# Performance work log

Hardware: AMD Instinct MI355X
Metric: run time of the kernel (lower is better)

## Reference

```python
import jax, jax.numpy as jnp
import numpy as np

B, N, C = 2, 1024, 256
HEADS, DH = 8, 32
INNER = HEADS * DH
L, P = 3, 9
FF = 512
DEPTH = 2
KNN_K = (16, 64)
SHAPES_NP = np.array([[128, 128], [64, 64], [32, 32]], np.int32)
LEN = int((SHAPES_NP[:, 0] * SHAPES_NP[:, 1]).sum())


def _ln(x, g, b, eps=1e-5):
    m = x.mean(-1, keepdims=True)
    v = ((x - m) ** 2).mean(-1, keepdims=True)
    return (x - m) * jax.lax.rsqrt(v + eps) * g + b


def _knn_gather(x, pos, k):
    # pos: [B,N,3]; self-KNN (includes self as nearest)
    sq = jnp.sum(pos ** 2, -1)
    d2 = sq[:, :, None] + sq[:, None, :] - 2.0 * jnp.einsum('bnd,bmd->bnm', pos, pos)
    _, idx = jax.lax.top_k(-d2, k)  # [B,N,k]
    return jax.vmap(lambda xb, ib: xb[ib])(x, idx)  # [B,N,k,C]


def _self_attn_knn(x, pos3d, Wq, Wkv, Wo, bo, k):
    Bq, Nq, _ = x.shape
    knn_x = _knn_gather(x, pos3d, k)
    q = (x @ Wq).reshape(Bq, Nq, HEADS, DH)
    kk, vv = jnp.split(knn_x @ Wkv, 2, -1)
    kk = kk.reshape(Bq, Nq, k, HEADS, DH)
    vv = vv.reshape(Bq, Nq, k, HEADS, DH)
    attn = jax.nn.softmax(jnp.einsum('bnhd,bnshd->bnhs', q, kk) * (DH ** -0.5), -1)
    out = jnp.einsum('bnhs,bnshd->bnhd', attn, vv).reshape(Bq, Nq, INNER)
    return out @ Wo + bo


def _bilinear(value_l, loc, Hl, Wl):
    # value_l: [B, Hl*Wl, HEADS, DH]; loc: [B,N,HEADS,P,2] normalized [0,1]
    # grid_sample(align_corners=False, padding_mode='zeros') semantics
    Bq, Nq, Hh, Pp, _ = loc.shape
    xf = loc[..., 0] * Wl - 0.5
    yf = loc[..., 1] * Hl - 0.5
    x0 = jnp.floor(xf)
    y0 = jnp.floor(yf)
    out = jnp.zeros((Bq, Nq, Hh, Pp, DH), value_l.dtype)
    for dy in (0.0, 1.0):
        for dx in (0.0, 1.0):
            ix, iy = x0 + dx, y0 + dy
            w = (1.0 - jnp.abs(xf - ix)) * (1.0 - jnp.abs(yf - iy))
            valid = (ix >= 0) & (ix <= Wl - 1) & (iy >= 0) & (iy <= Hl - 1)
            flat = (jnp.clip(iy, 0, Hl - 1) * Wl + jnp.clip(ix, 0, Wl - 1)).astype(jnp.int32)
            flat = flat.transpose(0, 1, 3, 2).reshape(Bq, Nq * Pp, Hh)
            idx = jnp.broadcast_to(flat[..., None], (Bq, Nq * Pp, Hh, DH))
            g = jnp.take_along_axis(value_l, idx, axis=1)
            g = g.reshape(Bq, Nq, Pp, Hh, DH).transpose(0, 1, 3, 2, 4)
            out = out + g * (w * valid)[..., None]
    return out


def _msdeform(q, ref, value_src, Wval, bval, Woff, boff, Waw, baw, Wo, bo):
    Bq, Nq, _ = q.shape
    value = (value_src @ Wval + bval).reshape(Bq, -1, HEADS, DH)
    off = (q @ Woff + boff).reshape(Bq, Nq, HEADS, L, P, 2)
    aw = jax.nn.softmax((q @ Waw + baw).reshape(Bq, Nq, HEADS, L * P), -1)
    aw = aw.reshape(Bq, Nq, HEADS, L, P)
    normalizer = jnp.asarray(SHAPES_NP[:, ::-1].copy(), jnp.float32)  # (W,H) per level
    loc = ref[:, :, None, :, None, :] + off / normalizer[None, None, None, :, None, :]
    out = jnp.zeros((Bq, Nq, HEADS, DH), q.dtype)
    start = 0
    for l in range(L):
        Hl, Wl = int(SHAPES_NP[l, 0]), int(SHAPES_NP[l, 1])
        v_l = value[:, start:start + Hl * Wl]
        samp = _bilinear(v_l, loc[:, :, :, l], Hl, Wl)  # [B,N,H,P,DH]
        out = out + jnp.einsum('bnhpd,bnhp->bnhd', samp, aw[:, :, :, l])
        start += Hl * Wl
    return out.reshape(Bq, Nq, INNER) @ Wo + bo


def _forward(x, src, center_pos, center_pos3d, W_pos, b_pos, ln1_g, ln1_b, ln2_g, ln2_b, ln3_g, ln3_b,
             Wq, Wkv, Wo_sa, bo_sa, Wval, bval, Woff, boff, Waw, baw, Wo_ca, bo_ca, W1, b1, W2, b2):
    cpe = center_pos[..., 0, :] @ W_pos + b_pos  # pos_embedding(center_pos[...,0,:])
    ref = center_pos  # [B,N,L,2]
    for i in range(DEPTH):
        h = _ln(x + cpe, ln1_g[i], ln1_b[i])
        x = x + _self_attn_knn(h, center_pos3d, Wq[i], Wkv[i], Wo_sa[i], bo_sa[i], KNN_K[i])
        q = _ln(x, ln2_g[i], ln2_b[i]) + cpe  # with_pos_embed(norm(x), query_pos)
        s = _ln(src, ln2_g[i], ln2_b[i])      # PreNorm applies same LN to src
        x = x + _msdeform(q, ref, s, Wval[i], bval[i], Woff[i], boff[i], Waw[i], baw[i], Wo_ca[i], bo_ca[i])
        hf = _ln(x, ln3_g[i], ln3_b[i])
        x = x + (jax.nn.gelu(hf @ W1[i] + b1[i], approximate=False) @ W2[i] + b2[i])
    return x


def setup_inputs():
    key = jax.random.key(0)
    ks = iter(jax.random.split(key, 64))
    rn = lambda shape, s=1.0: jax.random.normal(next(ks), shape, jnp.float32) * s
    w = 0.02
    starts = np.concatenate([[0], np.cumsum(SHAPES_NP[:, 0] * SHAPES_NP[:, 1])[:-1]]).astype(np.int32)
    return {
        'x': rn((B, N, C)),
        'src': rn((B, LEN, C)),
        'center_pos': jax.random.uniform(next(ks), (B, N, L, 2), jnp.float32),
        'center_pos3d': rn((B, N, 3)),
        'spatial_shapes': jnp.asarray(SHAPES_NP),
        'level_start_index': jnp.asarray(starts),
        'W_pos': rn((2, C), w), 'b_pos': jnp.zeros((C,), jnp.float32),
        'ln1_g': jnp.ones((DEPTH, C)), 'ln1_b': jnp.zeros((DEPTH, C)),
        'ln2_g': jnp.ones((DEPTH, C)), 'ln2_b': jnp.zeros((DEPTH, C)),
        'ln3_g': jnp.ones((DEPTH, C)), 'ln3_b': jnp.zeros((DEPTH, C)),
        'Wq': rn((DEPTH, C, INNER), w), 'Wkv': rn((DEPTH, C, 2 * INNER), w),
        'Wo_sa': rn((DEPTH, INNER, C), w), 'bo_sa': jnp.zeros((DEPTH, C)),
        'Wval': rn((DEPTH, C, INNER), w), 'bval': jnp.zeros((DEPTH, INNER)),
        'Woff': rn((DEPTH, C, HEADS * L * P * 2), w), 'boff': rn((DEPTH, HEADS * L * P * 2), w),
        'Waw': rn((DEPTH, C, HEADS * L * P), w), 'baw': jnp.zeros((DEPTH, HEADS * L * P)),
        'Wo_ca': rn((DEPTH, INNER, C), w), 'bo_ca': jnp.zeros((DEPTH, C)),
        'W1': rn((DEPTH, C, FF), w), 'b1': jnp.zeros((DEPTH, FF)),
        'W2': rn((DEPTH, FF, C), w), 'b2': jnp.zeros((DEPTH, C)),
    }


def reference(x, src, center_pos, center_pos3d, spatial_shapes, level_start_index, W_pos, b_pos,
              ln1_g, ln1_b, ln2_g, ln2_b, ln3_g, ln3_b, Wq, Wkv, Wo_sa, bo_sa,
              Wval, bval, Woff, boff, Waw, baw, Wo_ca, bo_ca, W1, b1, W2, b2):
    # spatial_shapes / level_start_index are fixed constants (SHAPES_NP) baked into the level loop.
    return _forward(x, src, center_pos, center_pos3d, W_pos, b_pos, ln1_g, ln1_b, ln2_g, ln2_b,
                    ln3_g, ln3_b, Wq, Wkv, Wo_sa, bo_sa, Wval, bval, Woff, boff, Waw, baw,
                    Wo_ca, bo_ca, W1, b1, W2, b2)
```

## Files before the change

### kernel.cpp

```cpp
#include <hip/hip_runtime.h>
#include <math.h>


#define DEV __device__ __forceinline__

typedef __attribute__((ext_vector_type(8))) short bf16x8;
typedef __attribute__((ext_vector_type(4))) float floatx4;

DEV float gelu_f(float v) { return 0.5f * v * (1.0f + erff(v * 0.7071067811865475f)); }

DEV unsigned short f2bf(float f) {
    unsigned u = __float_as_uint(f);
    return (unsigned short)((u + 0x7fffu + ((u >> 16) & 1u)) >> 16);
}

__global__ __launch_bounds__(256) void k_lnsrc(const float* __restrict__ x, unsigned short* __restrict__ out) {
    int wid = threadIdx.x >> 6, lane = threadIdx.x & 63;
    size_t row = (size_t)blockIdx.x * 4 + wid;
    float4 v = ((const float4*)(x + row * 256))[lane];
    float s = (v.x + v.y) + (v.z + v.w);
#pragma unroll
    for (int o = 32; o; o >>= 1) s += __shfl_xor(s, o);
    float mean = s * (1.0f / 256.0f);
    float dx = v.x - mean, dy = v.y - mean, dz = v.z - mean, dw = v.w - mean;
    float q = (dx * dx + dy * dy) + (dz * dz + dw * dw);
#pragma unroll
    for (int o = 32; o; o >>= 1) q += __shfl_xor(q, o);
    float rstd = 1.0f / sqrtf(q * (1.0f / 256.0f) + 1e-5f);
    ushort4 o4;
    o4.x = f2bf(dx * rstd);
    o4.y = f2bf(dy * rstd);
    o4.z = f2bf(dz * rstd);
    o4.w = f2bf(dw * rstd);
    ((ushort4*)(out + row * 256))[lane] = o4;
}

__global__ __launch_bounds__(256) void k_lnfused(const float* __restrict__ x, const float* pre, const float* post,
                                                 const float* __restrict__ g, const float* __restrict__ b,
                                                 unsigned short* __restrict__ out) {
    int wid = threadIdx.x >> 6, lane = threadIdx.x & 63;
    size_t row = (size_t)blockIdx.x * 4 + wid;
    float4 v = ((const float4*)(x + row * 256))[lane];
    if (pre) {
        float4 p = ((const float4*)(pre + row * 256))[lane];
        v.x += p.x; v.y += p.y; v.z += p.z; v.w += p.w;
    }
    float s = (v.x + v.y) + (v.z + v.w);
#pragma unroll
    for (int o = 32; o; o >>= 1) s += __shfl_xor(s, o);
    float mean = s * (1.0f / 256.0f);
    float dx = v.x - mean, dy = v.y - mean, dz = v.z - mean, dw = v.w - mean;
    float q = (dx * dx + dy * dy) + (dz * dz + dw * dw);
#pragma unroll
    for (int o = 32; o; o >>= 1) q += __shfl_xor(q, o);
    float rstd = 1.0f / sqrtf(q * (1.0f / 256.0f) + 1e-5f);
    float4 gg = ((const float4*)g)[lane], bb = ((const float4*)b)[lane];
    float4 o4;
    o4.x = dx * rstd * gg.x + bb.x;
    o4.y = dy * rstd * gg.y + bb.y;
    o4.z = dz * rstd * gg.z + bb.z;
    o4.w = dw * rstd * gg.w + bb.w;
    if (post) {
        float4 p = ((const float4*)(post + row * 256))[lane];
        o4.x += p.x; o4.y += p.y; o4.z += p.z; o4.w += p.w;
    }
    ushort4 u4;
    u4.x = f2bf(o4.x); u4.y = f2bf(o4.y); u4.z = f2bf(o4.z); u4.w = f2bf(o4.w);
    ((ushort4*)(out + row * 256))[lane] = u4;
}

__global__ __launch_bounds__(256) void k_cpe(const float* __restrict__ cpos, const float* __restrict__ Wp,
                                             const float* __restrict__ bp, float* __restrict__ cpe) {
    int bn = blockIdx.x, c = threadIdx.x;
    float px = cpos[(size_t)bn * 6 + 0], py = cpos[(size_t)bn * 6 + 1];
    cpe[(size_t)bn * 256 + c] = px * Wp[c] + py * Wp[256 + c] + bp[c];
}

__global__ __launch_bounds__(256) void k_knn2(const float* __restrict__ pos, int* __restrict__ k16,
                                              int* __restrict__ k64) {
    __shared__ float sp[3072];
    int b = blockIdx.x >> 8;
    int n0 = (blockIdx.x & 255) * 4;
    for (int t = threadIdx.x; t < 3072; t += 256) sp[t] = pos[(size_t)b * 3072 + t];
    __syncthreads();
    int wid = threadIdx.x >> 6, lane = threadIdx.x & 63;
    int n = n0 + wid;
    float qx = sp[n * 3], qy = sp[n * 3 + 1], qz = sp[n * 3 + 2];
    float sqn = (qx * qx + qy * qy) + qz * qz;
    unsigned du[16];
#pragma unroll
    for (int t = 0; t < 16; t++) {
        int m = t * 64 + lane;
        float mx = sp[m * 3], my = sp[m * 3 + 1], mz = sp[m * 3 + 2];
        float sqm = (mx * mx + my * my) + mz * mz;
        float dt = (qx * mx + qy * my) + qz * mz;
        float d2 = (sqn + sqm) - 2.0f * dt;
        unsigned u = __float_as_uint(d2);
        du[t] = (u & 0x80000000u) ? ~u : (u | 0x80000000u);
    }
    unsigned long long lmask = (1ull << lane) - 1ull;

    auto cnt_le = [&](unsigned p) {
        int c = 0;
#pragma unroll
        for (int t = 0; t < 16; t++) c += __popcll(__ballot(du[t] <= p));
        return c;
    };
    auto find_T = [&](int K) {
        unsigned lo = 0u, hi = 0xFFFFFFFFu;
        while (lo < hi) {
            unsigned mid = lo + ((hi - lo) >> 1);
            if (cnt_le(mid) >= K) hi = mid; else lo = mid + 1;
        }
        return hi;
    };
    auto emit = [&](int K, unsigned T, int* out) {
        int base = 0;
#pragma unroll
        for (int t = 0; t < 16; t++) {
            bool lt = du[t] < T;
            unsigned long long mk = __ballot(lt);
            if (lt) out[base + __popcll(mk & lmask)] = t * 64 + lane;
            base += __popcll(mk);
        }
        int need = K - base, eb = 0;
#pragma unroll
        for (int t = 0; t < 16; t++) {
            bool eq = du[t] == T;
            unsigned long long mk = __ballot(eq);
            if (eq) {
                int r = eb + __popcll(mk & lmask);
                if (r < need) out[base + r] = t * 64 + lane;
            }
            eb += __popcll(mk);
        }
    };
    unsigned T16 = find_T(16);
    emit(16, T16, k16 + ((size_t)b * 1024 + n) * 16);
    unsigned T64 = find_T(64);
    emit(64, T64, k64 + ((size_t)b * 1024 + n) * 64);
}

template <int KK>
__global__ __launch_bounds__(256) void k_attn(const float* __restrict__ hqkv, const int* __restrict__ kidx,
                                              unsigned short* __restrict__ out) {
    int bn = blockIdx.x;
    int b = bn >> 10;
    int tid = threadIdx.x;
    __shared__ float sq[256];
    __shared__ float sa[8][KK];
    __shared__ int si[KK];
    if (tid < KK) si[tid] = kidx[(size_t)bn * KK + tid];
    sq[tid] = hqkv[(size_t)bn * 768 + tid] * 0.17677669529663689f;
    __syncthreads();
    const float* kvb = hqkv + (size_t)b * 1024 * 768;
#pragma unroll
    for (int pair = tid; pair < 8 * KK; pair += 256) {
        int s = pair & (KK - 1);
        int h = pair / KK;
        const float4* kr = (const float4*)(kvb + (size_t)si[s] * 768 + 256 + h * 32);
        const float4* q4 = (const float4*)&sq[h * 32];
        float a0 = 0.f, a1 = 0.f, a2 = 0.f, a3 = 0.f;
#pragma unroll
        for (int e = 0; e < 8; e++) {
            float4 kv = kr[e];
            float4 qv = q4[e];
            a0 = fmaf(kv.x, qv.x, a0);
            a1 = fmaf(kv.y, qv.y, a1);
            a2 = fmaf(kv.z, qv.z, a2);
            a3 = fmaf(kv.w, qv.w, a3);
        }
        sa[h][s] = (a0 + a1) + (a2 + a3);
    }
    __syncthreads();
    int h = tid >> 5, d = tid & 31;
    float mx = -1e30f;
    for (int s = d; s < KK; s += 32) mx = fmaxf(mx, sa[h][s]);
#pragma unroll
    for (int o = 16; o; o >>= 1) mx = fmaxf(mx, __shfl_xor(mx, o, 32));
    float sum = 0.0f;
    for (int s = d; s < KK; s += 32) {
        float e = __expf(sa[h][s] - mx);
        sa[h][s] = e;
        sum += e;
    }
#pragma unroll
    for (int o = 16; o; o >>= 1) sum += __shfl_xor(sum, o, 32);
    float inv = 1.0f / sum;
    __syncthreads();
    float acc = 0.0f;
    for (int s = 0; s < KK; s++) {
        float vv = kvb[(size_t)si[s] * 768 + 512 + tid];
        acc += sa[h][s] * vv;
    }
    out[(size_t)bn * 256 + tid] = f2bf(acc * inv);
}

__global__ __launch_bounds__(256) void k_msdeform(const float* __restrict__ offaw, const float* __restrict__ cpos,
                                                  const unsigned short* __restrict__ value_d,
                                                  unsigned short* __restrict__ out) {
    int bn = blockIdx.x;
    int b = bn >> 10;
    int tid = threadIdx.x;
    __shared__ float aw[216];
    __shared__ uint2 meta[864];
    __shared__ float sacc[2][256];
    if (tid < 216) aw[tid] = offaw[(size_t)bn * 648 + 432 + tid];
    __syncthreads();
    if (tid < 8) {
        float mx = -1e30f;
        for (int p = 0; p < 27; p++) mx = fmaxf(mx, aw[tid * 27 + p]);
        float s = 0.0f;
        for (int p = 0; p < 27; p++) {
            float e = __expf(aw[tid * 27 + p] - mx);
            aw[tid * 27 + p] = e;
            s += e;
        }
        float inv = 1.0f / s;
        for (int p = 0; p < 27; p++) aw[tid * 27 + p] *= inv;
    }
    __syncthreads();
    if (tid < 216) {
        int h = tid / 27, lp = tid - h * 27;
        int l = lp / 9;
        const int dims[3] = {128, 64, 32};
        const int starts[3] = {0, 16384, 20480};
        int Wl = dims[l], st = starts[l];
        float rx = cpos[(size_t)bn * 6 + l * 2], ry = cpos[(size_t)bn * 6 + l * 2 + 1];
        float ox = offaw[(size_t)bn * 648 + h * 54 + lp * 2];
        float oy = offaw[(size_t)bn * 648 + h * 54 + lp * 2 + 1];
        float rw = 1.0f / (float)Wl;
        float xf = (rx + ox * rw) * (float)Wl - 0.5f;
        float yf = (ry + oy * rw) * (float)Wl - 0.5f;
        float x0 = floorf(xf), y0 = floorf(yf);
        float wgt = aw[tid];
#pragma unroll
        for (int c = 0; c < 4; c++) {
            float ix = x0 + (float)(c & 1), iy = y0 + (float)(c >> 1);
            float w = (1.0f - fabsf(xf - ix)) * (1.0f - fabsf(yf - iy));
            bool valid = (ix >= 0.0f) & (ix <= (float)(Wl - 1)) & (iy >= 0.0f) & (iy <= (float)(Wl - 1));
            uint2 m;
            if (valid && w != 0.0f) {
                m.x = __float_as_uint(w * wgt);
                m.y = (unsigned)((st + (int)iy * Wl + (int)ix) * 1024);
            } else {
                m.x = 0u;
                m.y = 0u;
            }
            meta[tid * 4 + c] = m;
        }
    }
    __syncthreads();
    int par = tid >> 7, h2 = (tid >> 4) & 7, d2 = tid & 15;
    const char* base = (const char*)(value_d + (size_t)b * 21504 * 512) + h2 * 64 + d2 * 4;
    const uint2* mp = &meta[h2 * 108 + par * 54];
    float a0 = 0.f, a1 = 0.f;
#pragma unroll
    for (int j = 0; j < 54; j++) {
        uint2 m = mp[j];
        unsigned v = *(const unsigned*)(base + m.y);
        float w = __uint_as_float(m.x);
        a0 = fmaf(w, __uint_as_float(v << 16), a0);
        a1 = fmaf(w, __uint_as_float(v & 0xffff0000u), a1);
    }
    int ch = h2 * 32 + d2 * 2;
    sacc[par][ch] = a0;
    sacc[par][ch + 1] = a1;
    __syncthreads();
    out[(size_t)bn * 256 + tid] = f2bf(sacc[0][tid] + sacc[1][tid]);
}

struct TJobs {
    const float* src[18];
    const float* gam[18];
    unsigned short* dst[18];
    int K[18];
    int N[18];
};
__global__ __launch_bounds__(256) void k_tw(TJobs j) {
    int job = blockIdx.z;
    int K = j.K[job], N = j.N[job];
    int nt = (N + 31) >> 5, kt = K >> 5;
    if ((int)blockIdx.x >= nt || (int)blockIdx.y >= kt) return;
    __shared__ float t[32][33];
    const float* W = j.src[job];
    const float* g = j.gam[job];
    unsigned short* Wt = j.dst[job];
    int x = threadIdx.x & 31, y = threadIdx.x >> 5;
    int n0 = blockIdx.x << 5, k0 = blockIdx.y << 5;
#pragma unroll
    for (int i = 0; i < 32; i += 8) {
        int n = n0 + x;
        t[y + i][x] = (n < N) ? W[(size_t)(k0 + y + i) * N + n] : 0.0f;
    }
    __syncthreads();
    float gv = g ? g[k0 + x] : 1.0f;
#pragma unroll
    for (int i = 0; i < 32; i += 8) {
        int n = n0 + y + i;
        if (n < N) Wt[(size_t)n * K + k0 + x] = f2bf(gv * t[x][y + i]);
    }
}

__global__ __launch_bounds__(256) void k_foldval(const float* __restrict__ ln2b, const float* __restrict__ Wval,
                                                 const float* __restrict__ bval, float* __restrict__ out) {
    int d = blockIdx.x, n = threadIdx.x;
    const float* W = Wval + (size_t)d * 65536 + n;
    const float* lb = ln2b + d * 256;
    float s = bval[d * 256 + n];
    for (int k = 0; k < 256; k++) s = fmaf(lb[k], W[(size_t)k * 256], s);
    out[d * 256 + n] = s;
}

template <int BN, int WGM, int WGN, bool BIAS, bool BIAS2, bool GELUF, bool RES, bool OBF16>
__global__ __launch_bounds__(256) void k_mgemm(const unsigned short* __restrict__ A,
                                               const unsigned short* __restrict__ Bt,
                                               const float* __restrict__ bias, const float* __restrict__ bias2,
                                               int bsplit, const float* __restrict__ res, void* __restrict__ Cout,
                                               int M, int K, int Ncol) {
    constexpr int BM = 64, BK = 32;
    constexpr int WAVE_M = BM / WGM, WAVE_N = BN / WGN;
    constexpr int FM = WAVE_M / 16, FN = WAVE_N / 16;
    constexpr int BUN = BN / 64;
    __shared__ __align__(16) short a_lds[4][BM][8];
    __shared__ __align__(16) short b_lds[4][BN][8];
    int tid = threadIdx.x;
    int am0 = blockIdx.y * BM, bn0 = blockIdx.x * BN;
    int ar = tid >> 2, akc = tid & 3;
    const unsigned short* Arow = A + (size_t)(am0 + ar) * K + akc * 8;
    int4 aq;
    int4 bq[BUN];
    int nsteps = K / BK;

    auto load_tile = [&](int k0) {
        aq = *(const int4*)(Arow + k0);
#pragma unroll
        for (int jj = 0; jj < BUN; jj++) {
            int u = tid + 256 * jj;
            int col = u >> 2, kc = u & 3;
            int gn = bn0 + col;
            if (gn < Ncol)
                bq[jj] = *(const int4*)(Bt + (size_t)gn * K + k0 + kc * 8);
            else
                bq[jj] = make_int4(0, 0, 0, 0);
        }
    };
    auto write_lds = [&]() {
        *(int4*)(&a_lds[akc][ar ^ akc][0]) = aq;
#pragma unroll
        for (int jj = 0; jj < BUN; jj++) {
            int u = tid + 256 * jj;
            int col = u >> 2, kc = u & 3;
            *(int4*)(&b_lds[kc][col ^ kc][0]) = bq[jj];
        }
    };
    int lane = tid & 63, wid = tid >> 6;
    int wm = wid / WGN, wn = wid % WGN;
    int fr = lane & 15, fkc = lane >> 4;
    floatx4 acc[FM][FN] = {};

    load_tile(0);
    for (int t = 0; t < nsteps; ++t) {
        if (t) __syncthreads();
        write_lds();
        __syncthreads();
        if (t + 1 < nsteps) load_tile((t + 1) * BK);
        bf16x8 af[FM], bf[FN];
#pragma unroll
        for (int m = 0; m < FM; m++) af[m] = *(const bf16x8*)(&a_lds[fkc][(wm * WAVE_M + m * 16 + fr) ^ fkc][0]);
#pragma unroll
        for (int n = 0; n < FN; n++) bf[n] = *(const bf16x8*)(&b_lds[fkc][(wn * WAVE_N + n * 16 + fr) ^ fkc][0]);
#pragma unroll
        for (int m = 0; m < FM; m++)
#pragma unroll
            for (int n = 0; n < FN; n++)
                acc[m][n] = __builtin_amdgcn_mfma_f32_16x16x32_bf16(af[m], bf[n], acc[m][n], 0, 0, 0);
    }
    int r4 = lane >> 4;
#pragma unroll
    for (int m = 0; m < FM; m++) {
        int row = am0 + wm * WAVE_M + m * 16 + r4 * 4;
#pragma unroll
        for (int n = 0; n < FN; n++) {
            int col = bn0 + wn * WAVE_N + n * 16 + fr;
            if (col < Ncol) {
                float bsc = 0.0f;
                if (BIAS) bsc = (BIAS2 && col >= bsplit) ? bias2[col - bsplit] : bias[col];
#pragma unroll
                for (int r = 0; r < 4; r++) {
                    size_t off = (size_t)(row + r) * Ncol + col;
                    float v = acc[m][n][r] + bsc;
                    if (GELUF) v = gelu_f(v);
                    if (RES) v += res[off];
                    if (OBF16)
                        ((unsigned short*)Cout)[off] = f2bf(v);
                    else
                        ((float*)Cout)[off] = v;
                }
            }
        }
    }
}

extern "C" void kernel_launch(void* const* d_in, const int* in_sizes, int n_in, void* d_out, int out_size,
                              void* d_ws, size_t ws_size, hipStream_t stream) {
    const float* xin = (const float*)d_in[0];
    const float* src = (const float*)d_in[1];
    const float* cpos = (const float*)d_in[2];
    const float* pos3 = (const float*)d_in[3];
    const float* Wpos = (const float*)d_in[6];
    const float* bpos = (const float*)d_in[7];
    const float* ln1g = (const float*)d_in[8];
    const float* ln1b = (const float*)d_in[9];
    const float* ln2g = (const float*)d_in[10];
    const float* ln2b = (const float*)d_in[11];
    const float* ln3g = (const float*)d_in[12];
    const float* ln3b = (const float*)d_in[13];
    const float* Wq = (const float*)d_in[14];
    const float* Wkv = (const float*)d_in[15];
    const float* Wosa = (const float*)d_in[16];
    const float* bosa = (const float*)d_in[17];
    const float* Wval = (const float*)d_in[18];
    const float* bval = (const float*)d_in[19];
    const float* Woff = (const float*)d_in[20];
    const float* boff = (const float*)d_in[21];
    const float* Waw = (const float*)d_in[22];
    const float* baw = (const float*)d_in[23];
    const float* Woca = (const float*)d_in[24];
    const float* boca = (const float*)d_in[25];
    const float* W1 = (const float*)d_in[26];
    const float* b1f = (const float*)d_in[27];
    const float* W2 = (const float*)d_in[28];
    const float* b2f = (const float*)d_in[29];
    float* x = (float*)d_out;

    float* ws = (float*)d_ws;
    float* cpe = ws;
    float* hqkv = cpe + 524288;
    float* offaw = hqkv + 1572864;
    float* bval2 = offaw + 1327104;
    unsigned short* lnout16 = (unsigned short*)(bval2 + 512);
    unsigned short* attn16 = lnout16 + 524288;
    unsigned short* cab16 = attn16 + 524288;
    unsigned short* ffmid16 = cab16 + 524288;
    unsigned short* srcn16 = ffmid16 + 1048576;
    unsigned short* value16 = srcn16 + 11010048;
    int* kidx16 = (int*)(value16 + 22020096);
    int* kidx64 = kidx16 + 32768;
    unsigned short* wt = (unsigned short*)(kidx64 + 131072);

    const size_t WT_STRIDE = 755712;
    const size_t O_WQKV = 0, O_WOSA = 196608, O_WOFFAW = 262144, O_WOCA = 428032,
                 O_W1 = 493568, O_W2 = 624640;
    unsigned short* wtval = wt + 2 * WT_STRIDE;

    TJobs tj;
    for (int d = 0; d < 2; d++) {
        unsigned short* wd = wt + (size_t)d * WT_STRIDE;
        int tb = d * 9;
        tj.src[tb + 0] = Wq + (size_t)d * 65536;    tj.gam[tb + 0] = nullptr;      tj.dst[tb + 0] = wd + O_WQKV;            tj.K[tb + 0] = 256; tj.N[tb + 0] = 256;
        tj.src[tb + 1] = Wkv + (size_t)d * 131072;  tj.gam[tb + 1] = nullptr;      tj.dst[tb + 1] = wd + O_WQKV + 65536;    tj.K[tb + 1] = 256; tj.N[tb + 1] = 512;
        tj.src[tb + 2] = Wosa + (size_t)d * 65536;  tj.gam[tb + 2] = nullptr;      tj.dst[tb + 2] = wd + O_WOSA;            tj.K[tb + 2] = 256; tj.N[tb + 2] = 256;
        tj.src[tb + 3] = Woff + (size_t)d * 110592; tj.gam[tb + 3] = nullptr;      tj.dst[tb + 3] = wd + O_WOFFAW;          tj.K[tb + 3] = 256; tj.N[tb + 3] = 432;
        tj.src[tb + 4] = Waw + (size_t)d * 55296;   tj.gam[tb + 4] = nullptr;      tj.dst[tb + 4] = wd + O_WOFFAW + 110592; tj.K[tb + 4] = 256; tj.N[tb + 4] = 216;
        tj.src[tb + 5] = Woca + (size_t)d * 65536;  tj.gam[tb + 5] = nullptr;      tj.dst[tb + 5] = wd + O_WOCA;            tj.K[tb + 5] = 256; tj.N[tb + 5] = 256;
        tj.src[tb + 6] = W1 + (size_t)d * 131072;   tj.gam[tb + 6] = nullptr;      tj.dst[tb + 6] = wd + O_W1;              tj.K[tb + 6] = 256; tj.N[tb + 6] = 512;
        tj.src[tb + 7] = W2 + (size_t)d * 131072;   tj.gam[tb + 7] = nullptr;      tj.dst[tb + 7] = wd + O_W2;              tj.K[tb + 7] = 512; tj.N[tb + 7] = 256;
        tj.src[tb + 8] = Wval + (size_t)d * 65536;  tj.gam[tb + 8] = ln2g + d * 256; tj.dst[tb + 8] = wtval + (size_t)d * 65536; tj.K[tb + 8] = 256; tj.N[tb + 8] = 256;
    }
    k_tw<<<dim3(16, 16, 18), 256, 0, stream>>>(tj);
    k_foldval<<<2, 256, 0, stream>>>(ln2b, Wval, bval, bval2);

    k_cpe<<<2048, 256, 0, stream>>>(cpos, Wpos, bpos, cpe);
    k_lnsrc<<<10752, 256, 0, stream>>>(src, srcn16);
    k_knn2<<<512, 256, 0, stream>>>(pos3, kidx16, kidx64);

    k_mgemm<256, 1, 4, true, false, false, false, true><<<dim3(2, 672), 256, 0, stream>>>(
        srcn16, wtval, bval2, nullptr, 0, nullptr, value16, 43008, 256, 512);

    for (int i = 0; i < 2; i++) {
        unsigned short* wd = wt + (size_t)i * WT_STRIDE;
        const float* xc = (i == 0) ? xin : x;
        k_lnfused<<<512, 256, 0, stream>>>(xc, cpe, nullptr, ln1g + i * 256, ln1b + i * 256, lnout16);
        k_mgemm<64, 2, 2, false, false, false, false, false><<<dim3(12, 32), 256, 0, stream>>>(
            lnout16, wd + O_WQKV, nullptr, nullptr, 0, nullptr, hqkv, 2048, 256, 768);
        if (i == 0)
            k_attn<16><<<2048, 256, 0, stream>>>(hqkv, kidx16, attn16);
        else
            k_attn<64><<<2048, 256, 0, stream>>>(hqkv, kidx64, attn16);
        k_mgemm<64, 2, 2, true, false, false, true, false><<<dim3(4, 32), 256, 0, stream>>>(
            attn16, wd + O_WOSA, bosa + i * 256, nullptr, 0, xc, x, 2048, 256, 256);

        k_lnfused<<<512, 256, 0, stream>>>(x, nullptr, cpe, ln2g + i * 256, ln2b + i * 256, lnout16);
        k_mgemm<64, 2, 2, true, true, false, false, false><<<dim3(11, 32), 256, 0, stream>>>(
            lnout16, wd + O_WOFFAW, boff + i * 432, baw + i * 216, 432, nullptr, offaw, 2048, 256, 648);
        k_msdeform<<<2048, 256, 0, stream>>>(offaw, cpos, value16 + (size_t)i * 256, cab16);
        k_mgemm<64, 2, 2, true, false, false, true, false><<<dim3(4, 32), 256, 0, stream>>>(
            cab16, wd + O_WOCA, boca + i * 256, nullptr, 0, x, x, 2048, 256, 256);

        k_lnfused<<<512, 256, 0, stream>>>(x, nullptr, nullptr, ln3g + i * 256, ln3b + i * 256, lnout16);
        k_mgemm<64, 2, 2, true, false, true, false, true><<<dim3(8, 32), 256, 0, stream>>>(
            lnout16, wd + O_W1, b1f + i * 512, nullptr, 0, nullptr, ffmid16, 2048, 256, 512);
        k_mgemm<64, 2, 2, true, false, false, true, false><<<dim3(4, 32), 256, 0, stream>>>(
            ffmid16, wd + O_W2, b2f + i * 256, nullptr, 0, x, x, 2048, 512, 256);
    }
}
```

Before: 237.8 us.

## Merge prologue kernels into one launch and shrink BM for N=256 GEMMs

Five independent prologue kernels (weight transpose, bias fold, position embedding, source layernorm, KNN) are merged into one kernel that dispatches on block index, which removes launch gaps and lets the pieces overlap. The GEMM template gains a BM parameter, and the three 256-column residual GEMMs use BM=32, which doubles their block count to fill more CUs. The cost is partially idle threads on A loads and a large heterogeneous grid whose blocks have uneven work.

```diff
diff --git a/kernel.cpp b/kernel.cpp
--- a/kernel.cpp
+++ b/kernel.cpp
@@ -12,27 +12,6 @@
 DEV unsigned short f2bf(float f) {
     unsigned u = __float_as_uint(f);
     return (unsigned short)((u + 0x7fffu + ((u >> 16) & 1u)) >> 16);
-}
-
-__global__ __launch_bounds__(256) void k_lnsrc(const float* __restrict__ x, unsigned short* __restrict__ out) {
-    int wid = threadIdx.x >> 6, lane = threadIdx.x & 63;
-    size_t row = (size_t)blockIdx.x * 4 + wid;
-    float4 v = ((const float4*)(x + row * 256))[lane];
-    float s = (v.x + v.y) + (v.z + v.w);
-#pragma unroll
-    for (int o = 32; o; o >>= 1) s += __shfl_xor(s, o);
-    float mean = s * (1.0f / 256.0f);
-    float dx = v.x - mean, dy = v.y - mean, dz = v.z - mean, dw = v.w - mean;
-    float q = (dx * dx + dy * dy) + (dz * dz + dw * dw);
-#pragma unroll
-    for (int o = 32; o; o >>= 1) q += __shfl_xor(q, o);
-    float rstd = 1.0f / sqrtf(q * (1.0f / 256.0f) + 1e-5f);
-    ushort4 o4;
-    o4.x = f2bf(dx * rstd);
-    o4.y = f2bf(dy * rstd);
-    o4.z = f2bf(dz * rstd);
-    o4.w = f2bf(dw * rstd);
-    ((ushort4*)(out + row * 256))[lane] = o4;
 }
 
 __global__ __launch_bounds__(256) void k_lnfused(const float* __restrict__ x, const float* pre, const float* post,
@@ -67,78 +46,6 @@
     ushort4 u4;
     u4.x = f2bf(o4.x); u4.y = f2bf(o4.y); u4.z = f2bf(o4.z); u4.w = f2bf(o4.w);
     ((ushort4*)(out + row * 256))[lane] = u4;
-}
-
-__global__ __launch_bounds__(256) void k_cpe(const float* __restrict__ cpos, const float* __restrict__ Wp,
-                                             const float* __restrict__ bp, float* __restrict__ cpe) {
-    int bn = blockIdx.x, c = threadIdx.x;
-    float px = cpos[(size_t)bn * 6 + 0], py = cpos[(size_t)bn * 6 + 1];
-    cpe[(size_t)bn * 256 + c] = px * Wp[c] + py * Wp[256 + c] + bp[c];
-}
-
-__global__ __launch_bounds__(256) void k_knn2(const float* __restrict__ pos, int* __restrict__ k16,
-                                              int* __restrict__ k64) {
-    __shared__ float sp[3072];
-    int b = blockIdx.x >> 8;
-    int n0 = (blockIdx.x & 255) * 4;
-    for (int t = threadIdx.x; t < 3072; t += 256) sp[t] = pos[(size_t)b * 3072 + t];
-    __syncthreads();
-    int wid = threadIdx.x >> 6, lane = threadIdx.x & 63;
-    int n = n0 + wid;
-    float qx = sp[n * 3], qy = sp[n * 3 + 1], qz = sp[n * 3 + 2];
-    float sqn = (qx * qx + qy * qy) + qz * qz;
-    unsigned du[16];
-#pragma unroll
-    for (int t = 0; t < 16; t++) {
-        int m = t * 64 + lane;
-        float mx = sp[m * 3], my = sp[m * 3 + 1], mz = sp[m * 3 + 2];
-        float sqm = (mx * mx + my * my) + mz * mz;
-        float dt = (qx * mx + qy * my) + qz * mz;
-        float d2 = (sqn + sqm) - 2.0f * dt;
-        unsigned u = __float_as_uint(d2);
-        du[t] = (u & 0x80000000u) ? ~u : (u | 0x80000000u);
-    }
-    unsigned long long lmask = (1ull << lane) - 1ull;
-
-    auto cnt_le = [&](unsigned p) {
-        int c = 0;
-#pragma unroll
-        for (int t = 0; t < 16; t++) c += __popcll(__ballot(du[t] <= p));
-        return c;
-    };
-    auto find_T = [&](int K) {
-        unsigned lo = 0u, hi = 0xFFFFFFFFu;
-        while (lo < hi) {
-            unsigned mid = lo + ((hi - lo) >> 1);
-            if (cnt_le(mid) >= K) hi = mid; else lo = mid + 1;
-        }
-        return hi;
-    };
-    auto emit = [&](int K, unsigned T, int* out) {
-        int base = 0;
-#pragma unroll
-        for (int t = 0; t < 16; t++) {
-            bool lt = du[t] < T;
-            unsigned long long mk = __ballot(lt);
-            if (lt) out[base + __popcll(mk & lmask)] = t * 64 + lane;
-            base += __popcll(mk);
-        }
-        int need = K - base, eb = 0;
-#pragma unroll
-        for (int t = 0; t < 16; t++) {
-            bool eq = du[t] == T;
-            unsigned long long mk = __ballot(eq);
-            if (eq) {
-                int r = eb + __popcll(mk & lmask);
-                if (r < need) out[base + r] = t * 64 + lane;
-            }
-            eb += __popcll(mk);
-        }
-    };
-    unsigned T16 = find_T(16);
-    emit(16, T16, k16 + ((size_t)b * 1024 + n) * 16);
-    unsigned T64 = find_T(64);
-    emit(64, T64, k64 + ((size_t)b * 1024 + n) * 64);
 }
 
 template <int KK>
@@ -277,63 +184,160 @@
     int K[18];
     int N[18];
 };
-__global__ __launch_bounds__(256) void k_tw(TJobs j) {
-    int job = blockIdx.z;
-    int K = j.K[job], N = j.N[job];
-    int nt = (N + 31) >> 5, kt = K >> 5;
-    if ((int)blockIdx.x >= nt || (int)blockIdx.y >= kt) return;
-    __shared__ float t[32][33];
-    const float* W = j.src[job];
-    const float* g = j.gam[job];
-    unsigned short* Wt = j.dst[job];
-    int x = threadIdx.x & 31, y = threadIdx.x >> 5;
-    int n0 = blockIdx.x << 5, k0 = blockIdx.y << 5;
-#pragma unroll
-    for (int i = 0; i < 32; i += 8) {
-        int n = n0 + x;
-        t[y + i][x] = (n < N) ? W[(size_t)(k0 + y + i) * N + n] : 0.0f;
-    }
-    __syncthreads();
-    float gv = g ? g[k0 + x] : 1.0f;
-#pragma unroll
-    for (int i = 0; i < 32; i += 8) {
-        int n = n0 + y + i;
-        if (n < N) Wt[(size_t)n * K + k0 + x] = f2bf(gv * t[x][y + i]);
-    }
-}
-
-__global__ __launch_bounds__(256) void k_foldval(const float* __restrict__ ln2b, const float* __restrict__ Wval,
-                                                 const float* __restrict__ bval, float* __restrict__ out) {
-    int d = blockIdx.x, n = threadIdx.x;
-    const float* W = Wval + (size_t)d * 65536 + n;
-    const float* lb = ln2b + d * 256;
-    float s = bval[d * 256 + n];
-    for (int k = 0; k < 256; k++) s = fmaf(lb[k], W[(size_t)k * 256], s);
-    out[d * 256 + n] = s;
-}
-
-template <int BN, int WGM, int WGN, bool BIAS, bool BIAS2, bool GELUF, bool RES, bool OBF16>
+__global__ __launch_bounds__(256) void k_pro(TJobs j, const float* __restrict__ cpos, const float* __restrict__ Wp,
+                                             const float* __restrict__ bp, float* __restrict__ cpe,
+                                             const float* __restrict__ ln2b, const float* __restrict__ Wval,
+                                             const float* __restrict__ bval, float* __restrict__ bval2,
+                                             const float* __restrict__ srcf, unsigned short* __restrict__ srcn,
+                                             const float* __restrict__ pos, int* __restrict__ k16,
+                                             int* __restrict__ k64) {
+    __shared__ float smem[3072];
+    int bid = blockIdx.x;
+    int tid = threadIdx.x;
+    if (bid < 4608) {
+        int job = bid >> 8, sub = bid & 255;
+        int bx = sub & 15, by = sub >> 4;
+        int K = j.K[job], N = j.N[job];
+        int nt = (N + 31) >> 5, kt = K >> 5;
+        if (bx >= nt || by >= kt) return;
+        float(*t)[33] = (float(*)[33])smem;
+        const float* W = j.src[job];
+        const float* g = j.gam[job];
+        unsigned short* Wt = j.dst[job];
+        int x = tid & 31, y = tid >> 5;
+        int n0 = bx << 5, k0 = by << 5;
+#pragma unroll
+        for (int i = 0; i < 32; i += 8) {
+            int n = n0 + x;
+            t[y + i][x] = (n < N) ? W[(size_t)(k0 + y + i) * N + n] : 0.0f;
+        }
+        __syncthreads();
+        float gv = g ? g[k0 + x] : 1.0f;
+#pragma unroll
+        for (int i = 0; i < 32; i += 8) {
+            int n = n0 + y + i;
+            if (n < N) Wt[(size_t)n * K + k0 + x] = f2bf(gv * t[x][y + i]);
+        }
+    } else if (bid < 6658) {
+        int bb = bid - 4608;
+        if (bb < 2048) {
+            float px = cpos[(size_t)bb * 6 + 0], py = cpos[(size_t)bb * 6 + 1];
+            cpe[(size_t)bb * 256 + tid] = px * Wp[tid] + py * Wp[256 + tid] + bp[tid];
+        } else {
+            int d = bb - 2048;
+            const float* W = Wval + (size_t)d * 65536 + tid;
+            const float* lb = ln2b + d * 256;
+            float s = bval[d * 256 + tid];
+            for (int k = 0; k < 256; k++) s = fmaf(lb[k], W[(size_t)k * 256], s);
+            bval2[d * 256 + tid] = s;
+        }
+    } else if (bid < 17410) {
+        int wid = tid >> 6, lane = tid & 63;
+        size_t row = (size_t)(bid - 6658) * 4 + wid;
+        float4 v = ((const float4*)(srcf + row * 256))[lane];
+        float s = (v.x + v.y) + (v.z + v.w);
+#pragma unroll
+        for (int o = 32; o; o >>= 1) s += __shfl_xor(s, o);
+        float mean = s * (1.0f / 256.0f);
+        float dx = v.x - mean, dy = v.y - mean, dz = v.z - mean, dw = v.w - mean;
+        float q = (dx * dx + dy * dy) + (dz * dz + dw * dw);
+#pragma unroll
+        for (int o = 32; o; o >>= 1) q += __shfl_xor(q, o);
+        float rstd = 1.0f / sqrtf(q * (1.0f / 256.0f) + 1e-5f);
+        ushort4 o4;
+        o4.x = f2bf(dx * rstd);
+        o4.y = f2bf(dy * rstd);
+        o4.z = f2bf(dz * rstd);
+        o4.w = f2bf(dw * rstd);
+        ((ushort4*)(srcn + row * 256))[lane] = o4;
+    } else {
+        int bb = bid - 17410;
+        float* sp = smem;
+        int b = bb >> 8;
+        int n0 = (bb & 255) * 4;
+        for (int t2 = tid; t2 < 3072; t2 += 256) sp[t2] = pos[(size_t)b * 3072 + t2];
+        __syncthreads();
+        int wid = tid >> 6, lane = tid & 63;
+        int n = n0 + wid;
+        float qx = sp[n * 3], qy = sp[n * 3 + 1], qz = sp[n * 3 + 2];
+        float sqn = (qx * qx + qy * qy) + qz * qz;
+        unsigned du[16];
+#pragma unroll
+        for (int t2 = 0; t2 < 16; t2++) {
+            int m = t2 * 64 + lane;
+            float mx = sp[m * 3], my = sp[m * 3 + 1], mz = sp[m * 3 + 2];
+            float sqm = (mx * mx + my * my) + mz * mz;
+            float dt = (qx * mx + qy * my) + qz * mz;
+            float d2 = (sqn + sqm) - 2.0f * dt;
+            unsigned u = __float_as_uint(d2);
+            du[t2] = (u & 0x80000000u) ? ~u : (u | 0x80000000u);
+        }
+        unsigned long long lmask = (1ull << lane) - 1ull;
+        auto cnt_le = [&](unsigned p) {
+            int c = 0;
+#pragma unroll
+            for (int t2 = 0; t2 < 16; t2++) c += __popcll(__ballot(du[t2] <= p));
+            return c;
+        };
+        auto find_T = [&](int K) {
+            unsigned lo = 0u, hi = 0xFFFFFFFFu;
+            while (lo < hi) {
+                unsigned mid = lo + ((hi - lo) >> 1);
+                if (cnt_le(mid) >= K) hi = mid; else lo = mid + 1;
+            }
+            return hi;
+        };
+        auto emit = [&](int K, unsigned T, int* out) {
+            int base = 0;
+#pragma unroll
+            for (int t2 = 0; t2 < 16; t2++) {
+                bool lt = du[t2] < T;
+                unsigned long long mk = __ballot(lt);
+                if (lt) out[base + __popcll(mk & lmask)] = t2 * 64 + lane;
+                base += __popcll(mk);
+            }
+            int need = K - base, eb = 0;
+#pragma unroll
+            for (int t2 = 0; t2 < 16; t2++) {
+                bool eq = du[t2] == T;
+                unsigned long long mk = __ballot(eq);
+                if (eq) {
+                    int r = eb + __popcll(mk & lmask);
+                    if (r < need) out[base + r] = t2 * 64 + lane;
+                }
+                eb += __popcll(mk);
+            }
+        };
+        unsigned T16 = find_T(16);
+        emit(16, T16, k16 + ((size_t)b * 1024 + n) * 16);
+        unsigned T64 = find_T(64);
+        emit(64, T64, k64 + ((size_t)b * 1024 + n) * 64);
+    }
+}
+
+template <int BM, int BN, int WGM, int WGN, bool BIAS, bool BIAS2, bool GELUF, bool RES, bool OBF16>
 __global__ __launch_bounds__(256) void k_mgemm(const unsigned short* __restrict__ A,
                                                const unsigned short* __restrict__ Bt,
                                                const float* __restrict__ bias, const float* __restrict__ bias2,
                                                int bsplit, const float* __restrict__ res, void* __restrict__ Cout,
                                                int M, int K, int Ncol) {
-    constexpr int BM = 64, BK = 32;
+    constexpr int BK = 32;
     constexpr int WAVE_M = BM / WGM, WAVE_N = BN / WGN;
     constexpr int FM = WAVE_M / 16, FN = WAVE_N / 16;
     constexpr int BUN = BN / 64;
+    constexpr int AUN = BM * 4;
     __shared__ __align__(16) short a_lds[4][BM][8];
     __shared__ __align__(16) short b_lds[4][BN][8];
     int tid = threadIdx.x;
     int am0 = blockIdx.y * BM, bn0 = blockIdx.x * BN;
     int ar = tid >> 2, akc = tid & 3;
-    const unsigned short* Arow = A + (size_t)(am0 + ar) * K + akc * 8;
+    const unsigned short* Arow = A + (size_t)(am0 + (ar & (BM - 1))) * K + akc * 8;
     int4 aq;
     int4 bq[BUN];
     int nsteps = K / BK;
 
     auto load_tile = [&](int k0) {
-        aq = *(const int4*)(Arow + k0);
+        if (AUN == 256 || tid < AUN) aq = *(const int4*)(Arow + k0);
 #pragma unroll
         for (int jj = 0; jj < BUN; jj++) {
             int u = tid + 256 * jj;
@@ -346,7 +350,7 @@
         }
     };
     auto write_lds = [&]() {
-        *(int4*)(&a_lds[akc][ar ^ akc][0]) = aq;
+        if (AUN == 256 || tid < AUN) *(int4*)(&a_lds[akc][ar ^ akc][0]) = aq;
 #pragma unroll
         for (int jj = 0; jj < BUN; jj++) {
             int u = tid + 256 * jj;
@@ -468,40 +472,36 @@
         tj.src[tb + 7] = W2 + (size_t)d * 131072;   tj.gam[tb + 7] = nullptr;      tj.dst[tb + 7] = wd + O_W2;              tj.K[tb + 7] = 512; tj.N[tb + 7] = 256;
         tj.src[tb + 8] = Wval + (size_t)d * 65536;  tj.gam[tb + 8] = ln2g + d * 256; tj.dst[tb + 8] = wtval + (size_t)d * 65536; tj.K[tb + 8] = 256; tj.N[tb + 8] = 256;
     }
-    k_tw<<<dim3(16, 16, 18), 256, 0, stream>>>(tj);
-    k_foldval<<<2, 256, 0, stream>>>(ln2b, Wval, bval, bval2);
-
-    k_cpe<<<2048, 256, 0, stream>>>(cpos, Wpos, bpos, cpe);
-    k_lnsrc<<<10752, 256, 0, stream>>>(src, srcn16);
-    k_knn2<<<512, 256, 0, stream>>>(pos3, kidx16, kidx64);
-
-    k_mgemm<256, 1, 4, true, false, false, false, true><<<dim3(2, 672), 256, 0, stream>>>(
+    k_pro<<<17922, 256, 0, stream>>>(tj, cpos, Wpos, bpos, cpe, ln2b, Wval, bval, bval2, src, srcn16, pos3,
+                                     kidx16, kidx64);
+
+    k_mgemm<64, 256, 1, 4, true, false, false, false, true><<<dim3(2, 672), 256, 0, stream>>>(
         srcn16, wtval, bval2, nullptr, 0, nullptr, value16, 43008, 256, 512);
 
     for (int i = 0; i < 2; i++) {
         unsigned short* wd = wt + (size_t)i * WT_STRIDE;
         const float* xc = (i == 0) ? xin : x;
         k_lnfused<<<512, 256, 0, stream>>>(xc, cpe, nullptr, ln1g + i * 256, ln1b + i * 256, lnout16);
-        k_mgemm<64, 2, 2, false, false, false, false, false><<<dim3(12, 32), 256, 0, stream>>>(
+        k_mgemm<64, 64, 2, 2, false, false, false, false, false><<<dim3(12, 32), 256, 0, stream>>>(
             lnout16, wd + O_WQKV, nullptr, nullptr, 0, nullptr, hqkv, 2048, 256, 768);
         if (i == 0)
             k_attn<16><<<2048, 256, 0, stream>>>(hqkv, kidx16, attn16);
         else
             k_attn<64><<<2048, 256, 0, stream>>>(hqkv, kidx64, attn16);
-        k_mgemm<64, 2, 2, true, false, false, true, false><<<dim3(4, 32), 256, 0, stream>>>(
+        k_mgemm<32, 64, 2, 2, true, false, false, true, false><<<dim3(4, 64), 256, 0, stream>>>(
             attn16, wd + O_WOSA, bosa + i * 256, nullptr, 0, xc, x, 2048, 256, 256);
 
         k_lnfused<<<512, 256, 0, stream>>>(x, nullptr, cpe, ln2g + i * 256, ln2b + i * 256, lnout16);
-        k_mgemm<64, 2, 2, true, true, false, false, false><<<dim3(11, 32), 256, 0, stream>>>(
+        k_mgemm<64, 64, 2, 2, true, true, false, false, false><<<dim3(11, 32), 256, 0, stream>>>(
             lnout16, wd + O_WOFFAW, boff + i * 432, baw + i * 216, 432, nullptr, offaw, 2048, 256, 648);
         k_msdeform<<<2048, 256, 0, stream>>>(offaw, cpos, value16 + (size_t)i * 256, cab16);
-        k_mgemm<64, 2, 2, true, false, false, true, false><<<dim3(4, 32), 256, 0, stream>>>(
+        k_mgemm<32, 64, 2, 2, true, false, false, true, false><<<dim3(4, 64), 256, 0, stream>>>(
             cab16, wd + O_WOCA, boca + i * 256, nullptr, 0, x, x, 2048, 256, 256);
 
         k_lnfused<<<512, 256, 0, stream>>>(x, nullptr, nullptr, ln3g + i * 256, ln3b + i * 256, lnout16);
-        k_mgemm<64, 2, 2, true, false, true, false, true><<<dim3(8, 32), 256, 0, stream>>>(
+        k_mgemm<64, 64, 2, 2, true, false, true, false, true><<<dim3(8, 32), 256, 0, stream>>>(
             lnout16, wd + O_W1, b1f + i * 512, nullptr, 0, nullptr, ffmid16, 2048, 256, 512);
-        k_mgemm<64, 2, 2, true, false, false, true, false><<<dim3(4, 32), 256, 0, stream>>>(
+        k_mgemm<32, 64, 2, 2, true, false, false, true, false><<<dim3(4, 64), 256, 0, stream>>>(
             ffmid16, wd + O_W2, b2f + i * 256, nullptr, 0, x, x, 2048, 512, 256);
     }
 }
```

Result: no change. 234.2 us (-1.5%).
